# Performance work log

Measured on AMD Instinct MI355X. Metric: run time of the kernel, lower is better.

Reference implementation:

```python
import jax, jax.numpy as jnp
import numpy as np

B, S, D, H, HID = 4, 1024, 1024, 16, 4096
DK = D // H
EPS = 1e-6


def _ln(x):
    # LayerNorm without affine, eps=1e-6
    mu = jnp.mean(x, axis=-1, keepdims=True)
    var = jnp.var(x, axis=-1, keepdims=True)
    return (x - mu) / jnp.sqrt(var + EPS)


def _lin(x, W, b):
    # torch Linear convention: W is [out, in]
    y = jnp.einsum('...i,oi->...o', x, W)
    return y + b if b is not None else y


def setup_inputs() -> dict:
    key = jax.random.key(0)
    ks = jax.random.split(key, 16)
    sc = lambda fan_in: 1.0 / np.sqrt(fan_in)
    inp = {
        'x': jax.random.normal(ks[0], (B, S, D), jnp.float32),
        'cond': jax.random.normal(ks[1], (B, 1, D), jnp.float32),
        'Wq': jax.random.normal(ks[2], (D, D), jnp.float32) * sc(D),
        'bq': jnp.zeros((D,), jnp.float32),
        'Wk': jax.random.normal(ks[3], (D, D), jnp.float32) * sc(D),
        'bk': jnp.zeros((D,), jnp.float32),
        'Wv': jax.random.normal(ks[4], (D, D), jnp.float32) * sc(D),
        'bv': jnp.zeros((D,), jnp.float32),
        'Wo': jax.random.normal(ks[5], (D, D), jnp.float32) * sc(D),
        'bo': jnp.zeros((D,), jnp.float32),
        'W1': jax.random.normal(ks[6], (HID, D), jnp.float32) * sc(D),
        'b1': jnp.zeros((HID,), jnp.float32),
        'W2': jax.random.normal(ks[7], (D, HID), jnp.float32) * sc(HID),
        'b2': jnp.zeros((D,), jnp.float32),
        'Wada': jax.random.normal(ks[8], (6 * D, D), jnp.float32) * sc(D),
        'bada': jnp.zeros((6 * D,), jnp.float32),
    }
    return inp


def reference(x, cond, Wq, bq, Wk, bk, Wv, bv, Wo, bo, W1, b1, W2, b2, Wada, bada):
    # adaLN modulation: SiLU -> Linear -> chunk 6 along last dim
    mod = _lin(jax.nn.silu(cond), Wada, bada)  # [B,1,6D]
    gama1, beta1, alpha1, gama2, beta2, alpha2 = jnp.split(mod, 6, axis=-1)

    # attention branch
    residual = x
    h = _ln(x) * (1.0 + beta1) + gama1  # modulate(shift=gama1, scale=beta1)
    q = _lin(h, Wq, bq).reshape(B, S, H, DK)
    k = _lin(h, Wk, bk).reshape(B, S, H, DK)
    v = _lin(h, Wv, bv).reshape(B, S, H, DK)
    scores = jnp.einsum('bqhd,bkhd->bhqk', q, k) / jnp.sqrt(jnp.float32(DK))
    probs = jax.nn.softmax(scores, axis=-1)
    attn = jnp.einsum('bhqk,bkhd->bqhd', probs, v).reshape(B, S, D)
    attn = _lin(attn, Wo, bo)
    x = residual + alpha1 * attn

    # MLP branch
    residual = x
    h = _ln(x) * (1.0 + beta2) + gama2
    h = _lin(h, W1, b1)
    h = jax.nn.gelu(h, approximate=False)  # torch nn.GELU default (erf)
    h = _lin(h, W2, b2)
    return residual + alpha2 * h
```

## Files before the change

### kernel.cpp

```cpp
#include <hip/hip_runtime.h>
#include <cstdint>

typedef __bf16 bf16_t;
typedef __bf16 bf16x4 __attribute__((ext_vector_type(4)));
typedef __bf16 bf16x8 __attribute__((ext_vector_type(8)));
typedef float f32x4 __attribute__((ext_vector_type(4)));

#define B_ 4
#define S_ 1024
#define D_ 1024
#define HID_ 4096
#define MEG (1u << 20)

static const size_t OFF_WBF  = 0;
static const size_t OFF_BQKV = 25165824;
static const size_t OFF_MOD  = 25178112;
static const size_t OFF_H    = 25276416;
static const size_t OFF_QKV  = 33665024;
static const size_t OFF_VT   = 58830848;
static const size_t OFF_ATTN = 67219456;
static const size_t OFF_X1   = 75608064;
static const size_t OFF_PART = 92385280;
static const size_t OFF_MLPH = 159494144;

__device__ __forceinline__ void async_copy16(const bf16_t* g, bf16_t* l) {
  __builtin_amdgcn_global_load_lds(
      (__attribute__((address_space(1))) void*)(g),
      (__attribute__((address_space(3))) void*)(l), 16, 0, 0);
}

__global__ __launch_bounds__(256) void convert_pack(
    const float* __restrict__ Wq, const float* __restrict__ Wk,
    const float* __restrict__ Wv, const float* __restrict__ Wo,
    const float* __restrict__ W1, const float* __restrict__ W2,
    const float* __restrict__ bq, const float* __restrict__ bk,
    const float* __restrict__ bv, bf16_t* __restrict__ wbf,
    float* __restrict__ bqkv) {
  const int y = blockIdx.y;
  if (y == 6) {
    int i = blockIdx.x * 256 + threadIdx.x;
    if (i < 3072)
      bqkv[i] = i < 1024 ? bq[i] : (i < 2048 ? bk[i - 1024] : bv[i - 2048]);
    return;
  }
  const float* src; bf16_t* dst; int n;
  switch (y) {
    case 0: src = Wq; dst = wbf;           n = MEG;     break;
    case 1: src = Wk; dst = wbf + MEG;     n = MEG;     break;
    case 2: src = Wv; dst = wbf + 2*MEG;   n = MEG;     break;
    case 3: src = Wo; dst = wbf + 3*MEG;   n = MEG;     break;
    case 4: src = W1; dst = wbf + 4*MEG;   n = 4*MEG;   break;
    default: src = W2; dst = wbf + 8*MEG;  n = 4*MEG;   break;
  }
  int idx = (blockIdx.x * 256 + threadIdx.x) * 4;
  if (idx < n) {
    float4 v = *(const float4*)(src + idx);
    bf16x4 pk;
    pk.x = (__bf16)v.x; pk.y = (__bf16)v.y; pk.z = (__bf16)v.z; pk.w = (__bf16)v.w;
    *(bf16x4*)(dst + idx) = pk;
  }
}

__global__ __launch_bounds__(256) void ada_mod(
    const float* __restrict__ cond, const float* __restrict__ Wada,
    const float* __restrict__ bada, float* __restrict__ mod) {
  const int wave = threadIdx.x >> 6, lane = threadIdx.x & 63;
  const int o = blockIdx.x * 4 + wave;
  const float* wr = Wada + (size_t)o * D_;
  float a0 = 0.f, a1 = 0.f, a2 = 0.f, a3 = 0.f;
#pragma unroll
  for (int l = 0; l < 16; l++) {
    int i = l * 64 + lane;
    float w = wr[i];
    float c0 = cond[i], c1 = cond[1024 + i], c2 = cond[2048 + i], c3 = cond[3072 + i];
    a0 += w * (c0 / (1.0f + __expf(-c0)));
    a1 += w * (c1 / (1.0f + __expf(-c1)));
    a2 += w * (c2 / (1.0f + __expf(-c2)));
    a3 += w * (c3 / (1.0f + __expf(-c3)));
  }
#pragma unroll
  for (int offs = 32; offs; offs >>= 1) {
    a0 += __shfl_xor(a0, offs);
    a1 += __shfl_xor(a1, offs);
    a2 += __shfl_xor(a2, offs);
    a3 += __shfl_xor(a3, offs);
  }
  if (lane == 0) {
    float bb = bada[o];
    mod[o]          = a0 + bb;
    mod[6144 + o]   = a1 + bb;
    mod[12288 + o]  = a2 + bb;
    mod[18432 + o]  = a3 + bb;
  }
}

__global__ __launch_bounds__(256) void ln_modulate(
    const float* __restrict__ X, const float* __restrict__ mod,
    bf16_t* __restrict__ H, int goff) {
  const int row = blockIdx.x;
  const int b = row >> 10;
  const int t = threadIdx.x;
  const float* xr = X + (size_t)row * D_;
  float4 xv = *(const float4*)(xr + t * 4);
  float s = xv.x + xv.y + xv.z + xv.w;
  float q = xv.x*xv.x + xv.y*xv.y + xv.z*xv.z + xv.w*xv.w;
  const int wave = t >> 6, lane = t & 63;
#pragma unroll
  for (int offs = 32; offs; offs >>= 1) {
    s += __shfl_down(s, offs);
    q += __shfl_down(q, offs);
  }
  __shared__ float sb[4][2];
  if (lane == 0) { sb[wave][0] = s; sb[wave][1] = q; }
  __syncthreads();
  float st = sb[0][0] + sb[1][0] + sb[2][0] + sb[3][0];
  float qt = sb[0][1] + sb[1][1] + sb[2][1] + sb[3][1];
  float mu = st * (1.0f / D_);
  float var = qt * (1.0f / D_) - mu * mu;
  float rstd = rsqrtf(var + 1e-6f);
  const float* mb = mod + (size_t)b * 6144 + goff;
  const int c = t * 4;
  float4 gm = *(const float4*)(mb + c);
  float4 bt = *(const float4*)(mb + 1024 + c);
  bf16x4 pk;
  pk.x = (__bf16)((xv.x - mu) * rstd * (1.0f + bt.x) + gm.x);
  pk.y = (__bf16)((xv.y - mu) * rstd * (1.0f + bt.y) + gm.y);
  pk.z = (__bf16)((xv.z - mu) * rstd * (1.0f + bt.z) + gm.z);
  pk.w = (__bf16)((xv.w - mu) * rstd * (1.0f + bt.w) + gm.w);
  *(bf16x4*)(H + (size_t)row * D_ + c) = pk;
}

__global__ __launch_bounds__(256) void transpose_v(
    const bf16_t* __restrict__ qkv, bf16_t* __restrict__ vT) {
  __shared__ bf16_t tile[64][65];
  const int bh = blockIdx.y;
  const int b = bh >> 4, hh = bh & 15;
  const int s0 = blockIdx.x * 64;
  const int t = threadIdx.x;
  const int tx = t & 63, ty = t >> 6;
  const bf16_t* src = qkv + (size_t)b * S_ * 3072 + 2048 + hh * 64;
  for (int r = ty; r < 64; r += 4)
    tile[r][tx] = src[(size_t)(s0 + r) * 3072 + tx];
  __syncthreads();
  bf16_t* dst = vT + (size_t)bh * 64 * 1024;
  for (int r = ty; r < 64; r += 4)
    dst[(size_t)r * 1024 + s0 + tx] = tile[tx][r];
}

__global__ __launch_bounds__(256, 4) void flash_attn(
    const bf16_t* __restrict__ qkv, const bf16_t* __restrict__ vT,
    bf16_t* __restrict__ attn) {
  __shared__ __align__(16) bf16_t Ks[2][64 * 64];
  __shared__ __align__(16) bf16_t Vs[2][64 * 64];
  __shared__ __align__(16) bf16_t Ps[4][16 * 64];

  const int t = threadIdx.x;
  const int wave = t >> 6, lane = t & 63;
  const int lm = lane & 15, quad = lane >> 4;
  const int bh = blockIdx.y;
  const int b = bh >> 4, hh = bh & 15;
  const int s0 = blockIdx.x * 64;

  const bf16_t* qbase = qkv + (size_t)b * S_ * 3072 + hh * 64;
  const bf16_t* kbase = qbase + 1024;
  const bf16_t* vbase = vT + (size_t)bh * (64 * 1024);

  const int row0 = t >> 3;
  const int cg = (t & 7) ^ (row0 & 7);
  const int o0 = t * 8, o1 = 2048 + t * 8;

  async_copy16(qbase + (size_t)(s0 + row0) * 3072 + cg * 8, &Ks[1][o0]);
  async_copy16(qbase + (size_t)(s0 + 32 + row0) * 3072 + cg * 8, &Ks[1][o1]);
  async_copy16(kbase + (size_t)row0 * 3072 + cg * 8, &Ks[0][o0]);
  async_copy16(kbase + (size_t)(32 + row0) * 3072 + cg * 8, &Ks[0][o1]);
  async_copy16(vbase + (size_t)row0 * 1024 + cg * 8, &Vs[0][o0]);
  async_copy16(vbase + (size_t)(32 + row0) * 1024 + cg * 8, &Vs[0][o1]);
  __syncthreads();

  bf16x8 aq0, aq1;
  {
    const int rq = wave * 16 + lm;
    const int rb = lm & 7;
    aq0 = *(const bf16x8*)&Ks[1][rq * 64 + (quad ^ rb) * 8];
    aq1 = *(const bf16x8*)&Ks[1][rq * 64 + ((4 + quad) ^ rb) * 8];
  }
  __syncthreads();

  f32x4 accO[4] = {};
  float mrow[4], lrow[4];
#pragma unroll
  for (int r = 0; r < 4; r++) { mrow[r] = -1e30f; lrow[r] = 0.f; }

  const float SC = 0.18033688f;
  bf16_t* Pw = Ps[wave];
  const int rb = lm & 7;

  for (int tt = 0; tt < 16; ++tt) {
    const int cur = tt & 1;
    if (tt < 15) {
      const int nb = cur ^ 1;
      const int k0n = (tt + 1) << 6;
      async_copy16(kbase + (size_t)(k0n + row0) * 3072 + cg * 8, &Ks[nb][o0]);
      async_copy16(kbase + (size_t)(k0n + 32 + row0) * 3072 + cg * 8, &Ks[nb][o1]);
      async_copy16(vbase + (size_t)row0 * 1024 + k0n + cg * 8, &Vs[nb][o0]);
      async_copy16(vbase + (size_t)(32 + row0) * 1024 + k0n + cg * 8, &Vs[nb][o1]);
    }

    f32x4 accS[4] = {};
    __builtin_amdgcn_s_setprio(1);
#pragma unroll
    for (int ni = 0; ni < 4; ni++) {
      const int rk = ni * 16 + lm;
      bf16x8 b0 = *(const bf16x8*)&Ks[cur][rk * 64 + ((quad ^ rb)) * 8];
      bf16x8 b1 = *(const bf16x8*)&Ks[cur][rk * 64 + (((4 + quad) ^ rb)) * 8];
      accS[ni] = __builtin_amdgcn_mfma_f32_16x16x32_bf16(aq0, b0, accS[ni], 0, 0, 0);
      accS[ni] = __builtin_amdgcn_mfma_f32_16x16x32_bf16(aq1, b1, accS[ni], 0, 0, 0);
    }
    __builtin_amdgcn_s_setprio(0);

    float alpha[4];
#pragma unroll
    for (int r = 0; r < 4; r++) {
      float mx = fmaxf(fmaxf(accS[0][r], accS[1][r]),
                       fmaxf(accS[2][r], accS[3][r])) * SC;
      mx = fmaxf(mx, __shfl_xor(mx, 1));
      mx = fmaxf(mx, __shfl_xor(mx, 2));
      mx = fmaxf(mx, __shfl_xor(mx, 4));
      mx = fmaxf(mx, __shfl_xor(mx, 8));
      float mnew = fmaxf(mrow[r], mx);
      alpha[r] = exp2f(mrow[r] - mnew);
      mrow[r] = mnew;
      float sum = 0.f;
#pragma unroll
      for (int ni = 0; ni < 4; ni++) {
        float p = exp2f(accS[ni][r] * SC - mnew);
        accS[ni][r] = p;
        sum += p;
      }
      sum += __shfl_xor(sum, 1);
      sum += __shfl_xor(sum, 2);
      sum += __shfl_xor(sum, 4);
      sum += __shfl_xor(sum, 8);
      lrow[r] = lrow[r] * alpha[r] + sum;
    }
#pragma unroll
    for (int di = 0; di < 4; di++)
#pragma unroll
      for (int r = 0; r < 4; r++) accO[di][r] *= alpha[r];

#pragma unroll
    for (int ni = 0; ni < 4; ni++)
#pragma unroll
      for (int r = 0; r < 4; r++) {
        int prow = quad * 4 + r;
        int col = ni * 16 + lm;
        Pw[prow * 64 + (((col >> 3) ^ (prow & 7)) << 3) + (col & 7)] =
            (__bf16)accS[ni][r];
      }

    {
      bf16x8 ap0 = *(const bf16x8*)&Pw[lm * 64 + ((quad ^ rb)) * 8];
      bf16x8 ap1 = *(const bf16x8*)&Pw[lm * 64 + (((4 + quad) ^ rb)) * 8];
      __builtin_amdgcn_s_setprio(1);
#pragma unroll
      for (int di = 0; di < 4; di++) {
        const int rv = di * 16 + lm;
        bf16x8 v0 = *(const bf16x8*)&Vs[cur][rv * 64 + ((quad ^ rb)) * 8];
        bf16x8 v1 = *(const bf16x8*)&Vs[cur][rv * 64 + (((4 + quad) ^ rb)) * 8];
        accO[di] = __builtin_amdgcn_mfma_f32_16x16x32_bf16(ap0, v0, accO[di], 0, 0, 0);
        accO[di] = __builtin_amdgcn_mfma_f32_16x16x32_bf16(ap1, v1, accO[di], 0, 0, 0);
      }
      __builtin_amdgcn_s_setprio(0);
    }
    __syncthreads();
  }

#pragma unroll
  for (int r = 0; r < 4; r++) {
    float inv = 1.0f / lrow[r];
    int prow = quad * 4 + r;
#pragma unroll
    for (int di = 0; di < 4; di++) {
      int col = di * 16 + lm;
      int cph = (col >> 3) ^ (prow & 7);
      Pw[prow * 64 + cph * 8 + (col & 7)] = (__bf16)(accO[di][r] * inv);
    }
  }
  bf16_t* abase = attn + (size_t)b * S_ * 1024 +
                  (size_t)(s0 + wave * 16) * 1024 + hh * 64;
#pragma unroll
  for (int it = 0; it < 2; it++) {
    int slot = it * 64 + lane;
    int orow = slot >> 3;
    int gc = slot & 7;
    int cph = gc ^ (orow & 7);
    bf16x8 val = *(const bf16x8*)&Pw[orow * 64 + cph * 8];
    *(bf16x8*)(abase + (size_t)orow * 1024 + gc * 8) = val;
  }
}

template <int EPI>
__global__ __launch_bounds__(256) void gemm_bt(
    const bf16_t* __restrict__ A, int lda, long long sAz,
    const bf16_t* __restrict__ B, int ldb, long long sBz,
    void* __restrict__ Cv, int ldc, long long sCz,
    int M, int N, int K,
    const float* __restrict__ bias,
    float scale) {
  __shared__ __align__(16) bf16_t As[2][128 * 32];
  __shared__ __align__(16) bf16_t Bs[2][128 * 32];

  const int z = blockIdx.z;
  A += (size_t)z * sAz;
  B += (size_t)z * sBz;

  {
    int d = blockIdx.x + gridDim.x * blockIdx.y;
    int xcd = d & 7, sId = d >> 3;
    int qq = sId & 31, panel = sId >> 5;
    const int bx = panel * 8 + (qq >> 2);
    const int by = xcd * 4 + (qq & 3);
    const int t = threadIdx.x;
    const int wave = t >> 6;
    const int lane = t & 63;
    const int lm = lane & 15;
    const int quad = lane >> 4;
    const int wr = wave >> 1;
    const int wc = wave & 1;

    const int m0 = by * 128;
    const int n0 = bx * 128;

    f32x4 acc[4][4] = {};

    const int srow = t >> 2;
    const int gch = (t & 3) ^ ((srow >> 1) & 3);
    const int lds_off = t * 8;
    const bf16_t* Ap0 = A + (size_t)(m0 + srow) * lda + gch * 8;
    const bf16_t* Ap1 = A + (size_t)(m0 + 64 + srow) * lda + gch * 8;
    const bf16_t* Bp0 = B + (size_t)(n0 + srow) * ldb + gch * 8;
    const bf16_t* Bp1 = B + (size_t)(n0 + 64 + srow) * ldb + gch * 8;

    const int sOff = (quad ^ ((lm >> 1) & 3)) * 8;

    const int niter = K >> 5;
    async_copy16(Ap0, &As[0][lds_off]);
    async_copy16(Ap1, &As[0][2048 + lds_off]);
    async_copy16(Bp0, &Bs[0][lds_off]);
    async_copy16(Bp1, &Bs[0][2048 + lds_off]);

    for (int it = 0; it < niter; ++it) {
      asm volatile("s_waitcnt vmcnt(0)\n\ts_barrier" ::: "memory");
      if (it + 1 < niter) {
        const int ko = (it + 1) << 5;
        const int nb = (it + 1) & 1;
        async_copy16(Ap0 + ko, &As[nb][lds_off]);
        async_copy16(Ap1 + ko, &As[nb][2048 + lds_off]);
        async_copy16(Bp0 + ko, &Bs[nb][lds_off]);
        async_copy16(Bp1 + ko, &Bs[nb][2048 + lds_off]);
      }
      const int cb = it & 1;
      bf16x8 af[4], bfr[4];
#pragma unroll
      for (int i = 0; i < 4; i++) {
        af[i] = *(const bf16x8*)&As[cb][(wr * 64 + i * 16 + lm) * 32 + sOff];
        bfr[i] = *(const bf16x8*)&Bs[cb][(wc * 64 + i * 16 + lm) * 32 + sOff];
      }
#pragma unroll
      for (int mi = 0; mi < 4; mi++)
#pragma unroll
        for (int ni = 0; ni < 4; ni++)
          acc[mi][ni] = __builtin_amdgcn_mfma_f32_16x16x32_bf16(
              af[mi], bfr[ni], acc[mi][ni], 0, 0, 0);
    }

    const size_t cz = (size_t)z * sCz;
#pragma unroll
    for (int mi = 0; mi < 4; mi++) {
#pragma unroll
      for (int ni = 0; ni < 4; ni++) {
#pragma unroll
        for (int r = 0; r < 4; r++) {
          int row = m0 + wr * 64 + mi * 16 + quad * 4 + r;
          int col = n0 + wc * 64 + ni * 16 + lm;
          float v = acc[mi][ni][r];
          size_t idx = cz + (size_t)row * ldc + col;
          if (EPI == 1) {
            ((float*)Cv)[idx] = v * scale;
          } else if (EPI == 0) {
            if (bias) v += bias[col];
            ((bf16_t*)Cv)[idx] = (__bf16)v;
          } else if (EPI == 3) {
            v += bias[col];
            float u = 1.5957691216f * (v + 0.044715f * v * v * v);
            float g = v / (1.0f + __expf(-u));
            ((bf16_t*)Cv)[idx] = (__bf16)g;
          }
        }
      }
    }
  }
}

__global__ __launch_bounds__(256) void reduce_ln(
    const float* __restrict__ part, const float* __restrict__ x,
    const float* __restrict__ bo, const float* __restrict__ mod,
    float* __restrict__ x1, bf16_t* __restrict__ h) {
  const int row = blockIdx.x;
  const int b = row >> 10;
  const int t = threadIdx.x;
  const int c = t * 4;
  const size_t idx = (size_t)row * 1024 + c;
  float4 p0 = *(const float4*)(part + idx);
  float4 p1 = *(const float4*)(part + 4194304 + idx);
  float4 bb = *(const float4*)(bo + c);
  float4 al = *(const float4*)(mod + (size_t)b * 6144 + 2048 + c);
  float4 xs = *(const float4*)(x + idx);
  float4 xv;
  xv.x = xs.x + al.x * (p0.x + p1.x + bb.x);
  xv.y = xs.y + al.y * (p0.y + p1.y + bb.y);
  xv.z = xs.z + al.z * (p0.z + p1.z + bb.z);
  xv.w = xs.w + al.w * (p0.w + p1.w + bb.w);
  *(float4*)(x1 + idx) = xv;

  float s = xv.x + xv.y + xv.z + xv.w;
  float q = xv.x*xv.x + xv.y*xv.y + xv.z*xv.z + xv.w*xv.w;
  const int wave = t >> 6, lane = t & 63;
#pragma unroll
  for (int offs = 32; offs; offs >>= 1) {
    s += __shfl_down(s, offs);
    q += __shfl_down(q, offs);
  }
  __shared__ float sb[4][2];
  if (lane == 0) { sb[wave][0] = s; sb[wave][1] = q; }
  __syncthreads();
  float st = sb[0][0] + sb[1][0] + sb[2][0] + sb[3][0];
  float qt = sb[0][1] + sb[1][1] + sb[2][1] + sb[3][1];
  float mu = st * (1.0f / D_);
  float var = qt * (1.0f / D_) - mu * mu;
  float rstd = rsqrtf(var + 1e-6f);
  const float* mb = mod + (size_t)b * 6144 + 3072;
  float4 gm = *(const float4*)(mb + c);
  float4 bt = *(const float4*)(mb + 1024 + c);
  bf16x4 pk;
  pk.x = (__bf16)((xv.x - mu) * rstd * (1.0f + bt.x) + gm.x);
  pk.y = (__bf16)((xv.y - mu) * rstd * (1.0f + bt.y) + gm.y);
  pk.z = (__bf16)((xv.z - mu) * rstd * (1.0f + bt.z) + gm.z);
  pk.w = (__bf16)((xv.w - mu) * rstd * (1.0f + bt.w) + gm.w);
  *(bf16x4*)(h + idx) = pk;
}

__global__ __launch_bounds__(256) void reduce_w2(
    const float* __restrict__ part, const float* __restrict__ x1,
    const float* __restrict__ b2, const float* __restrict__ mod,
    float* __restrict__ out) {
  const int idx = (blockIdx.x * 256 + threadIdx.x) * 4;
  const int col = idx & 1023;
  const int row = idx >> 10;
  const int b = row >> 10;
  float4 s0 = *(const float4*)(part + idx);
  float4 s1 = *(const float4*)(part + 4194304 + idx);
  float4 bb = *(const float4*)(b2 + col);
  float4 al = *(const float4*)(mod + (size_t)b * 6144 + 5120 + col);
  float4 rs = *(const float4*)(x1 + idx);
  float4 o;
  o.x = rs.x + al.x * (s0.x + s1.x + bb.x);
  o.y = rs.y + al.y * (s0.y + s1.y + bb.y);
  o.z = rs.z + al.z * (s0.z + s1.z + bb.z);
  o.w = rs.w + al.w * (s0.w + s1.w + bb.w);
  *(float4*)(out + idx) = o;
}

extern "C" void kernel_launch(void* const* d_in, const int* in_sizes, int n_in,
                              void* d_out, int out_size, void* d_ws, size_t ws_size,
                              hipStream_t stream) {
  (void)in_sizes; (void)n_in; (void)out_size; (void)ws_size;
  const float* x    = (const float*)d_in[0];
  const float* cond = (const float*)d_in[1];
  const float* Wq   = (const float*)d_in[2];
  const float* bq   = (const float*)d_in[3];
  const float* Wk   = (const float*)d_in[4];
  const float* bk   = (const float*)d_in[5];
  const float* Wv   = (const float*)d_in[6];
  const float* bv   = (const float*)d_in[7];
  const float* Wo   = (const float*)d_in[8];
  const float* bo   = (const float*)d_in[9];
  const float* W1   = (const float*)d_in[10];
  const float* b1   = (const float*)d_in[11];
  const float* W2   = (const float*)d_in[12];
  const float* b2   = (const float*)d_in[13];
  const float* Wada = (const float*)d_in[14];
  const float* bada = (const float*)d_in[15];

  uint8_t* ws = (uint8_t*)d_ws;
  bf16_t* wbf   = (bf16_t*)(ws + OFF_WBF);
  float*  bqkv  = (float*)(ws + OFF_BQKV);
  float*  mod   = (float*)(ws + OFF_MOD);
  bf16_t* h     = (bf16_t*)(ws + OFF_H);
  bf16_t* qkv   = (bf16_t*)(ws + OFF_QKV);
  bf16_t* vT    = (bf16_t*)(ws + OFF_VT);
  bf16_t* attn  = (bf16_t*)(ws + OFF_ATTN);
  float*  x1    = (float*)(ws + OFF_X1);
  float*  part  = (float*)(ws + OFF_PART);
  bf16_t* mlph  = (bf16_t*)(ws + OFF_MLPH);
  float* out = (float*)d_out;

  convert_pack<<<dim3(4096, 7, 1), 256, 0, stream>>>(Wq, Wk, Wv, Wo, W1, W2,
                                                     bq, bk, bv, wbf, bqkv);
  ada_mod<<<1536, 256, 0, stream>>>(cond, Wada, bada, mod);
  ln_modulate<<<4096, 256, 0, stream>>>(x, mod, h, 0);
  gemm_bt<0><<<dim3(24, 32, 1), 256, 0, stream>>>(
      h, 1024, 0, wbf, 1024, 0, qkv, 3072, 0, 4096, 3072, 1024,
      bqkv, 1.f);
  transpose_v<<<dim3(16, 64, 1), 256, 0, stream>>>(qkv, vT);
  flash_attn<<<dim3(16, 64, 1), 256, 0, stream>>>(qkv, vT, attn);

  gemm_bt<1><<<dim3(8, 32, 2), 256, 0, stream>>>(
      attn, 1024, 512, wbf + (size_t)3 * MEG, 1024, 512, part, 1024, 4194304,
      4096, 1024, 512, nullptr, 1.f);
  reduce_ln<<<4096, 256, 0, stream>>>(part, x, bo, mod, x1, h);

  gemm_bt<3><<<dim3(32, 32, 1), 256, 0, stream>>>(
      h, 1024, 0, wbf + (size_t)4 * MEG, 1024, 0, mlph, 4096, 0,
      4096, 4096, 1024, b1, 1.f);
  gemm_bt<1><<<dim3(8, 32, 2), 256, 0, stream>>>(
      mlph, 4096, 2048, wbf + (size_t)8 * MEG, 4096, 2048, part, 1024, 4194304,
      4096, 1024, 2048, nullptr, 1.f);
  reduce_w2<<<4096, 256, 0, stream>>>(part, x1, b2, mod, out);
}
```

Measured before the change: 406.2 us.

## Widen flash-attention KV tile to 128 and skip rescale when max grows little

The flash attention loop now processes 128 keys per iteration instead of 64, which halves the number of barriers and softmax reduction passes. Shared memory for K, V and P doubles, and the min-blocks launch bound is dropped. A lazy rescale is added: the running max and the output/sum rescale are updated only when some row's new max exceeds the old one by more than 8 (log2 units), with the check done wave-uniformly. This saves exp and multiply work, but intermediate exponentials can reach up to 2^8, and higher LDS and register use may lower occupancy.

New measurement: 404.4 us. About the same (-0.5%).

```diff
diff --git a/kernel.cpp b/kernel.cpp
--- a/kernel.cpp
+++ b/kernel.cpp
@@ -147,12 +147,12 @@
     dst[(size_t)r * 1024 + s0 + tx] = tile[tx][r];
 }
 
-__global__ __launch_bounds__(256, 4) void flash_attn(
+__global__ __launch_bounds__(256) void flash_attn(
     const bf16_t* __restrict__ qkv, const bf16_t* __restrict__ vT,
     bf16_t* __restrict__ attn) {
-  __shared__ __align__(16) bf16_t Ks[2][64 * 64];
-  __shared__ __align__(16) bf16_t Vs[2][64 * 64];
-  __shared__ __align__(16) bf16_t Ps[4][16 * 64];
+  __shared__ __align__(16) bf16_t Ks[2][2][64 * 64];
+  __shared__ __align__(16) bf16_t Vs[2][2][64 * 64];
+  __shared__ __align__(16) bf16_t Ps[4][2][16 * 64];
 
   const int t = threadIdx.x;
   const int wave = t >> 6, lane = t & 63;
@@ -168,21 +168,28 @@
   const int row0 = t >> 3;
   const int cg = (t & 7) ^ (row0 & 7);
   const int o0 = t * 8, o1 = 2048 + t * 8;
-
-  async_copy16(qbase + (size_t)(s0 + row0) * 3072 + cg * 8, &Ks[1][o0]);
-  async_copy16(qbase + (size_t)(s0 + 32 + row0) * 3072 + cg * 8, &Ks[1][o1]);
-  async_copy16(kbase + (size_t)row0 * 3072 + cg * 8, &Ks[0][o0]);
-  async_copy16(kbase + (size_t)(32 + row0) * 3072 + cg * 8, &Ks[0][o1]);
-  async_copy16(vbase + (size_t)row0 * 1024 + cg * 8, &Vs[0][o0]);
-  async_copy16(vbase + (size_t)(32 + row0) * 1024 + cg * 8, &Vs[0][o1]);
+  const bf16_t* kr = kbase + (size_t)row0 * 3072 + cg * 8;
+  const bf16_t* vr0 = vbase + (size_t)row0 * 1024 + cg * 8;
+  const bf16_t* vr1 = vbase + (size_t)(32 + row0) * 1024 + cg * 8;
+
+  async_copy16(qbase + (size_t)(s0 + row0) * 3072 + cg * 8, &Ks[1][0][o0]);
+  async_copy16(qbase + (size_t)(s0 + 32 + row0) * 3072 + cg * 8, &Ks[1][0][o1]);
+  async_copy16(kr, &Ks[0][0][o0]);
+  async_copy16(kr + (size_t)32 * 3072, &Ks[0][0][o1]);
+  async_copy16(kr + (size_t)64 * 3072, &Ks[0][1][o0]);
+  async_copy16(kr + (size_t)96 * 3072, &Ks[0][1][o1]);
+  async_copy16(vr0, &Vs[0][0][o0]);
+  async_copy16(vr1, &Vs[0][0][o1]);
+  async_copy16(vr0 + 64, &Vs[0][1][o0]);
+  async_copy16(vr1 + 64, &Vs[0][1][o1]);
   __syncthreads();
 
   bf16x8 aq0, aq1;
   {
     const int rq = wave * 16 + lm;
-    const int rb = lm & 7;
-    aq0 = *(const bf16x8*)&Ks[1][rq * 64 + (quad ^ rb) * 8];
-    aq1 = *(const bf16x8*)&Ks[1][rq * 64 + ((4 + quad) ^ rb) * 8];
+    const int rbq = lm & 7;
+    aq0 = *(const bf16x8*)&Ks[1][0][rq * 64 + (quad ^ rbq) * 8];
+    aq1 = *(const bf16x8*)&Ks[1][0][rq * 64 + ((4 + quad) ^ rbq) * 8];
   }
   __syncthreads();
 
@@ -192,86 +199,109 @@
   for (int r = 0; r < 4; r++) { mrow[r] = -1e30f; lrow[r] = 0.f; }
 
   const float SC = 0.18033688f;
-  bf16_t* Pw = Ps[wave];
   const int rb = lm & 7;
 
-  for (int tt = 0; tt < 16; ++tt) {
+  for (int tt = 0; tt < 8; ++tt) {
     const int cur = tt & 1;
-    if (tt < 15) {
+    if (tt < 7) {
       const int nb = cur ^ 1;
-      const int k0n = (tt + 1) << 6;
-      async_copy16(kbase + (size_t)(k0n + row0) * 3072 + cg * 8, &Ks[nb][o0]);
-      async_copy16(kbase + (size_t)(k0n + 32 + row0) * 3072 + cg * 8, &Ks[nb][o1]);
-      async_copy16(vbase + (size_t)row0 * 1024 + k0n + cg * 8, &Vs[nb][o0]);
-      async_copy16(vbase + (size_t)(32 + row0) * 1024 + k0n + cg * 8, &Vs[nb][o1]);
-    }
-
-    f32x4 accS[4] = {};
+      const size_t k0n = (size_t)(tt + 1) << 7;
+      const bf16_t* kn = kr + k0n * 3072;
+      async_copy16(kn, &Ks[nb][0][o0]);
+      async_copy16(kn + (size_t)32 * 3072, &Ks[nb][0][o1]);
+      async_copy16(kn + (size_t)64 * 3072, &Ks[nb][1][o0]);
+      async_copy16(kn + (size_t)96 * 3072, &Ks[nb][1][o1]);
+      async_copy16(vr0 + k0n, &Vs[nb][0][o0]);
+      async_copy16(vr1 + k0n, &Vs[nb][0][o1]);
+      async_copy16(vr0 + k0n + 64, &Vs[nb][1][o0]);
+      async_copy16(vr1 + k0n + 64, &Vs[nb][1][o1]);
+    }
+
+    f32x4 accS[8];
+#pragma unroll
+    for (int j = 0; j < 8; j++) accS[j] = (f32x4){0.f, 0.f, 0.f, 0.f};
     __builtin_amdgcn_s_setprio(1);
 #pragma unroll
-    for (int ni = 0; ni < 4; ni++) {
-      const int rk = ni * 16 + lm;
-      bf16x8 b0 = *(const bf16x8*)&Ks[cur][rk * 64 + ((quad ^ rb)) * 8];
-      bf16x8 b1 = *(const bf16x8*)&Ks[cur][rk * 64 + (((4 + quad) ^ rb)) * 8];
-      accS[ni] = __builtin_amdgcn_mfma_f32_16x16x32_bf16(aq0, b0, accS[ni], 0, 0, 0);
-      accS[ni] = __builtin_amdgcn_mfma_f32_16x16x32_bf16(aq1, b1, accS[ni], 0, 0, 0);
+    for (int h = 0; h < 2; h++) {
+#pragma unroll
+      for (int ni = 0; ni < 4; ni++) {
+        const int rk = ni * 16 + lm;
+        bf16x8 b0 = *(const bf16x8*)&Ks[cur][h][rk * 64 + ((quad ^ rb)) * 8];
+        bf16x8 b1 = *(const bf16x8*)&Ks[cur][h][rk * 64 + (((4 + quad) ^ rb)) * 8];
+        f32x4 a = accS[h * 4 + ni];
+        a = __builtin_amdgcn_mfma_f32_16x16x32_bf16(aq0, b0, a, 0, 0, 0);
+        a = __builtin_amdgcn_mfma_f32_16x16x32_bf16(aq1, b1, a, 0, 0, 0);
+        accS[h * 4 + ni] = a;
+      }
     }
     __builtin_amdgcn_s_setprio(0);
 
-    float alpha[4];
+    float mx[4];
 #pragma unroll
     for (int r = 0; r < 4; r++) {
-      float mx = fmaxf(fmaxf(accS[0][r], accS[1][r]),
-                       fmaxf(accS[2][r], accS[3][r])) * SC;
-      mx = fmaxf(mx, __shfl_xor(mx, 1));
-      mx = fmaxf(mx, __shfl_xor(mx, 2));
-      mx = fmaxf(mx, __shfl_xor(mx, 4));
-      mx = fmaxf(mx, __shfl_xor(mx, 8));
-      float mnew = fmaxf(mrow[r], mx);
-      alpha[r] = exp2f(mrow[r] - mnew);
-      mrow[r] = mnew;
+      float m0 = fmaxf(fmaxf(accS[0][r], accS[1][r]), fmaxf(accS[2][r], accS[3][r]));
+      float m1 = fmaxf(fmaxf(accS[4][r], accS[5][r]), fmaxf(accS[6][r], accS[7][r]));
+      float m8 = fmaxf(m0, m1);
+      m8 = fmaxf(m8, __shfl_xor(m8, 1));
+      m8 = fmaxf(m8, __shfl_xor(m8, 2));
+      m8 = fmaxf(m8, __shfl_xor(m8, 4));
+      m8 = fmaxf(m8, __shfl_xor(m8, 8));
+      mx[r] = m8 * SC;
+    }
+    bool ok = (mx[0] - mrow[0] <= 8.0f) && (mx[1] - mrow[1] <= 8.0f) &&
+              (mx[2] - mrow[2] <= 8.0f) && (mx[3] - mrow[3] <= 8.0f);
+    if (!__all(ok)) {
+#pragma unroll
+      for (int r = 0; r < 4; r++) {
+        float mnew = fmaxf(mrow[r], mx[r]);
+        float al = exp2f(mrow[r] - mnew);
+        mrow[r] = mnew;
+        lrow[r] *= al;
+#pragma unroll
+        for (int di = 0; di < 4; di++) accO[di][r] *= al;
+      }
+    }
+#pragma unroll
+    for (int r = 0; r < 4; r++) {
       float sum = 0.f;
 #pragma unroll
-      for (int ni = 0; ni < 4; ni++) {
-        float p = exp2f(accS[ni][r] * SC - mnew);
-        accS[ni][r] = p;
+      for (int j = 0; j < 8; j++) {
+        float p = exp2f(accS[j][r] * SC - mrow[r]);
+        accS[j][r] = p;
         sum += p;
       }
       sum += __shfl_xor(sum, 1);
       sum += __shfl_xor(sum, 2);
       sum += __shfl_xor(sum, 4);
       sum += __shfl_xor(sum, 8);
-      lrow[r] = lrow[r] * alpha[r] + sum;
-    }
-#pragma unroll
-    for (int di = 0; di < 4; di++)
-#pragma unroll
-      for (int r = 0; r < 4; r++) accO[di][r] *= alpha[r];
-
-#pragma unroll
-    for (int ni = 0; ni < 4; ni++)
+      lrow[r] += sum;
+    }
+
+#pragma unroll
+    for (int j = 0; j < 8; j++)
 #pragma unroll
       for (int r = 0; r < 4; r++) {
         int prow = quad * 4 + r;
-        int col = ni * 16 + lm;
-        Pw[prow * 64 + (((col >> 3) ^ (prow & 7)) << 3) + (col & 7)] =
-            (__bf16)accS[ni][r];
-      }
-
-    {
-      bf16x8 ap0 = *(const bf16x8*)&Pw[lm * 64 + ((quad ^ rb)) * 8];
-      bf16x8 ap1 = *(const bf16x8*)&Pw[lm * 64 + (((4 + quad) ^ rb)) * 8];
-      __builtin_amdgcn_s_setprio(1);
+        int c = (j & 3) * 16 + lm;
+        Ps[wave][j >> 2][prow * 64 + (((c >> 3) ^ (prow & 7)) << 3) + (c & 7)] =
+            (__bf16)accS[j][r];
+      }
+
+    __builtin_amdgcn_s_setprio(1);
+#pragma unroll
+    for (int ks = 0; ks < 4; ks++) {
+      const int half = ks >> 1, loc = ks & 1;
+      bf16x8 ap = *(const bf16x8*)&Ps[wave][half]
+          [lm * 64 + (((loc * 4 + quad) ^ rb)) * 8];
 #pragma unroll
       for (int di = 0; di < 4; di++) {
         const int rv = di * 16 + lm;
-        bf16x8 v0 = *(const bf16x8*)&Vs[cur][rv * 64 + ((quad ^ rb)) * 8];
-        bf16x8 v1 = *(const bf16x8*)&Vs[cur][rv * 64 + (((4 + quad) ^ rb)) * 8];
-        accO[di] = __builtin_amdgcn_mfma_f32_16x16x32_bf16(ap0, v0, accO[di], 0, 0, 0);
-        accO[di] = __builtin_amdgcn_mfma_f32_16x16x32_bf16(ap1, v1, accO[di], 0, 0, 0);
-      }
-      __builtin_amdgcn_s_setprio(0);
-    }
+        bf16x8 vv = *(const bf16x8*)&Vs[cur][half]
+            [rv * 64 + (((loc * 4 + quad) ^ rb)) * 8];
+        accO[di] = __builtin_amdgcn_mfma_f32_16x16x32_bf16(ap, vv, accO[di], 0, 0, 0);
+      }
+    }
+    __builtin_amdgcn_s_setprio(0);
     __syncthreads();
   }
 
@@ -283,7 +313,7 @@
     for (int di = 0; di < 4; di++) {
       int col = di * 16 + lm;
       int cph = (col >> 3) ^ (prow & 7);
-      Pw[prow * 64 + cph * 8 + (col & 7)] = (__bf16)(accO[di][r] * inv);
+      Ps[wave][0][prow * 64 + cph * 8 + (col & 7)] = (__bf16)(accO[di][r] * inv);
     }
   }
   bf16_t* abase = attn + (size_t)b * S_ * 1024 +
@@ -294,7 +324,7 @@
     int orow = slot >> 3;
     int gc = slot & 7;
     int cph = gc ^ (orow & 7);
-    bf16x8 val = *(const bf16x8*)&Pw[orow * 64 + cph * 8];
+    bf16x8 val = *(const bf16x8*)&Ps[wave][0][orow * 64 + cph * 8];
     *(bf16x8*)(abase + (size_t)orow * 1024 + gc * 8) = val;
   }
 }
```
